# Optimization experiments

Hardware: AMD Instinct MI355X
Metric: run time of the kernel (lower is better)

The kernel has to match this reference:

```python
import jax, jax.numpy as jnp
import numpy as np

LN_EPS = 1e-5
DIM = 128
HEADS = 6
DIM_HEAD = 32
INNER = HEADS * DIM_HEAD          # 192
FF_INNER = int(DIM * 4 * 2 / 3)   # 341 (GEGLU inner dim)
LOCAL_WINDOW = 200
CACHE = 3
COMPRESS = 2
TW = LOCAL_WINDOW + CACHE         # 203
B = 2
T = 12800                         # 32 chunks of 400


def layer_norm(x, w, b):
    m = x.mean(-1, keepdims=True)
    v = ((x - m) ** 2).mean(-1, keepdims=True)
    return (x - m) / jnp.sqrt(v + LN_EPS) * w + b


def apply_rotary(q, k):
    # q, k: (b, h, n, d); standard half-rotation rotary over absolute positions
    d = q.shape[-1]
    n = q.shape[2]
    inv_freq = 1.0 / (10000.0 ** (jnp.arange(0, d, 2, dtype=jnp.float32) / d))
    freqs = jnp.arange(n, dtype=jnp.float32)[:, None] * inv_freq  # (n, d/2)
    emb = jnp.concatenate([freqs, freqs], axis=-1)                # (n, d)
    cos = jnp.cos(emb).astype(q.dtype)
    sin = jnp.sin(emb).astype(q.dtype)

    def rot_half(x):
        x1, x2 = jnp.split(x, 2, axis=-1)
        return jnp.concatenate([-x2, x1], axis=-1)

    rope = lambda x: x * cos + rot_half(x) * sin
    return rope(q), rope(k)


def local_attention(q, k, v, w):
    # causal local attention, look_backward=1 window, look_forward=0 (lucidrains LocalAttention)
    b, h, n, d = q.shape
    nw = n // w
    q, k = apply_rotary(q, k)
    qw = q.reshape(b, h, nw, w, d)

    def look_around(x):
        xw = x.reshape(b, h, nw, w, d)
        prev = jnp.pad(xw[:, :, :-1], ((0, 0), (0, 0), (1, 0), (0, 0), (0, 0)))
        return jnp.concatenate([prev, xw], axis=3)  # (b,h,nw,2w,d)

    kw = look_around(k)
    vw = look_around(v)

    t = jnp.arange(n).reshape(nw, w)
    tk_prev = jnp.pad(t[:-1], ((1, 0), (0, 0)), constant_values=-1)
    tk = jnp.concatenate([tk_prev, t], axis=1)  # (nw, 2w); -1 marks padding
    mask = (t[:, :, None] >= tk[:, None, :]) & (tk[:, None, :] >= 0)  # (nw, w, 2w)

    sim = jnp.einsum('bhwid,bhwjd->bhwij', qw, kw) * (d ** -0.5)
    neg = jnp.finfo(sim.dtype).min
    sim = jnp.where(mask[None, None], sim, neg)
    attn = jax.nn.softmax(sim, axis=-1)
    out = jnp.einsum('bhwij,bhwjd->bhwid', attn, vw)
    return out.reshape(b, h, n, d)


def local_mha(x, ln_w, ln_b, wqkv, wo, window):
    h = layer_norm(x, ln_w, ln_b)
    qkv = h @ wqkv                       # (b, n, 3*INNER)
    q, k, v = jnp.split(qkv, 3, axis=-1)

    def split_heads(t):
        bb, n, _ = t.shape
        return t.reshape(bb, n, HEADS, DIM_HEAD).transpose(0, 2, 1, 3)

    out = local_attention(split_heads(q), split_heads(k), split_heads(v), window)
    bb, hh, n, d = out.shape
    out = out.transpose(0, 2, 1, 3).reshape(bb, n, hh * d)
    return out @ wo


def feed_forward(x, ln_w, ln_b, w1, w2):
    h = layer_norm(x, ln_w, ln_b) @ w1   # (b, n, 2*FF_INNER)
    a, gate = jnp.split(h, 2, axis=-1)
    return (a * jax.nn.gelu(gate, approximate=False)) @ w2


def local_trans(x, ln1_w, ln1_b, wqkv, wo, ln2_w, ln2_b, w1, w2, window):
    n_layers = ln1_w.shape[0]
    for i in range(n_layers):
        x = x + local_mha(x, ln1_w[i], ln1_b[i], wqkv[i], wo[i], window)
        x = x + feed_forward(x, ln2_w[i], ln2_b[i], w1[i], w2[i])
    return x


def setup_inputs() -> dict:
    key = jax.random.key(0)
    ks = jax.random.split(key, 16)
    std = 0.02
    rn = lambda k, shape: jax.random.normal(k, shape, dtype=jnp.float32) * std
    inp = {
        'x': jax.random.normal(ks[0], (B, DIM, T), dtype=jnp.float32),
        'cache_token': jax.random.normal(ks[1], (1, CACHE * COMPRESS, DIM), dtype=jnp.float32),
    }
    ki = 2
    for g in ('dt', 'lt'):
        inp[g + '_ln1_w'] = jnp.ones((2, DIM), jnp.float32)
        inp[g + '_ln1_b'] = jnp.zeros((2, DIM), jnp.float32)
        inp[g + '_wqkv'] = rn(ks[ki], (2, DIM, 3 * INNER)); ki += 1
        inp[g + '_wo'] = rn(ks[ki], (2, INNER, DIM)); ki += 1
        inp[g + '_ln2_w'] = jnp.ones((2, DIM), jnp.float32)
        inp[g + '_ln2_b'] = jnp.zeros((2, DIM), jnp.float32)
        inp[g + '_w1'] = rn(ks[ki], (2, DIM, 2 * FF_INNER)); ki += 1
        inp[g + '_w2'] = rn(ks[ki], (2, FF_INNER, DIM)); ki += 1
    inp['conv_w'] = rn(ks[ki], (DIM, DIM, COMPRESS)); ki += 1
    inp['conv_b'] = jnp.zeros((DIM,), jnp.float32)
    return inp


def reference(x, cache_token,
              dt_ln1_w, dt_ln1_b, dt_wqkv, dt_wo, dt_ln2_w, dt_ln2_b, dt_w1, dt_w2,
              lt_ln1_w, lt_ln1_b, lt_wqkv, lt_wo, lt_ln2_w, lt_ln2_b, lt_w1, lt_w2,
              conv_w, conv_b):
    feat = x.transpose(0, 2, 1)                     # (B, T, C)
    b, t, c = feat.shape
    chunk = LOCAL_WINDOW * COMPRESS                 # 400
    nchunks = t // chunk
    feat = feat.reshape(b, nchunks, chunk, c)
    ct = jnp.broadcast_to(cache_token[:, None], (b, nchunks, CACHE * COMPRESS, c))
    feat = jnp.concatenate([ct, feat], axis=2)      # interleave cache tokens per chunk
    feat = feat.reshape(b, nchunks * (chunk + CACHE * COMPRESS), c)

    # DownTrans: 2-layer local transformer (window 406) + strided conv compress
    feat = local_trans(feat, dt_ln1_w, dt_ln1_b, dt_wqkv, dt_wo,
                       dt_ln2_w, dt_ln2_b, dt_w1, dt_w2, TW * COMPRESS)
    y = jax.lax.conv_general_dilated(
        feat.transpose(0, 2, 1), conv_w, (COMPRESS,), 'VALID',
        dimension_numbers=('NCH', 'OIH', 'NCH')) + conv_b[None, :, None]
    feat = y.transpose(0, 2, 1)                     # (B, n/2, C)

    # remaining depth-2 local transformer (window 203)
    feat = local_trans(feat, lt_ln1_w, lt_ln1_b, lt_wqkv, lt_wo,
                       lt_ln2_w, lt_ln2_b, lt_w1, lt_w2, TW)
    return feat
```

## Files before the change

### kernel.cpp

```cpp
#include <hip/hip_runtime.h>
#include <cstdint>
#include <cstddef>

#define DIM    128
#define HEADS  6
#define INNER  192
#define QKV3   576
#define FFI    341
#define FF2    682
#define GGP    352
#define BATCH  2
#define T_IN   12800
#define N1     12992
#define N2     6496
#define ROWS1  (BATCH * N1)
#define ROWS2  (BATCH * N2)
#define W_DT   406
#define W_LT   203

typedef unsigned short ushortT;
typedef unsigned int u32;
typedef __bf16 bf16x8 __attribute__((ext_vector_type(8)));
typedef float f32x4 __attribute__((ext_vector_type(4)));

__device__ __forceinline__ f32x4 mfma16(bf16x8 a, bf16x8 b, f32x4 c) {
  return __builtin_amdgcn_mfma_f32_16x16x32_bf16(a, b, c, 0, 0, 0);
}
__device__ __forceinline__ ushortT f2bf(float x) {
  union { __bf16 b; ushortT u; } c; c.b = (__bf16)x; return c.u;
}
__device__ __forceinline__ void async_copy16(const ushortT* g, ushortT* l) {
  __builtin_amdgcn_global_load_lds(
      (const __attribute__((address_space(1))) unsigned int*)g,
      (__attribute__((address_space(3))) unsigned int*)l, 16, 0, 0);
}

static constexpr size_t OF_FEAT = 0;
static constexpr size_t OF_H    = OF_FEAT + (size_t)ROWS1 * DIM;
static constexpr size_t OF_QKH  = OF_H + (size_t)ROWS1 * DIM / 2;
static constexpr size_t SZ_QKH  = ((size_t)(ROWS1 + 128) * 384) / 2;
static constexpr size_t OF_AO   = OF_QKH + SZ_QKH;
static constexpr size_t OF_VT   = OF_AO + (size_t)ROWS1 * INNER / 2;
static constexpr size_t SZ_VT   = ((size_t)384 * (N1 + 128)) / 2;
static constexpr size_t OF_GG   = OF_VT + SZ_VT;
static constexpr size_t OF_F2   = OF_GG + (size_t)ROWS1 * GGP / 2;
static constexpr size_t OF_WT   = OF_F2 + (size_t)ROWS2 * DIM;
static constexpr size_t WT_QKV = 0;
static constexpr size_t WT_WO  = 81920;
static constexpr size_t WT_W1  = 106496;
static constexpr size_t WT_W2  = 204800;
static constexpr size_t WT_SET = 249856;
static constexpr size_t OF_CW  = OF_WT + (4 * WT_SET) / 2 + 64;
static constexpr size_t OF_ROPE = OF_CW + (128 * 256) / 2 + 64;
static constexpr size_t OF_H2  = OF_ROPE + (size_t)N1 * 32;

__global__ void build_feat_kernel(const float* __restrict__ x,
                                  const float* __restrict__ cache,
                                  float* __restrict__ feat) {
  int idx = blockIdx.x * 256 + threadIdx.x;
  if (idx >= ROWS1 * DIM) return;
  int d = idx & 127;
  int row = idx >> 7;
  int b = row / N1;
  int i = row - b * N1;
  int c = i / 406;
  int j = i - c * 406;
  float v;
  if (j < 6) v = cache[j * DIM + d];
  else       v = x[((size_t)b * DIM + d) * T_IN + (c * 400 + j - 6)];
  feat[idx] = v;
}

__global__ __launch_bounds__(256) void ln_kernel(const float* __restrict__ x,
                                                 ushortT* __restrict__ y,
                                                 const float* __restrict__ w,
                                                 const float* __restrict__ bb,
                                                 int rows) {
  int row = blockIdx.x * 4 + (threadIdx.x >> 6);
  if (row >= rows) return;
  int lane = threadIdx.x & 63;
  const float* xr = x + (size_t)row * DIM;
  float2 v = *(const float2*)(xr + lane * 2);
  float s = v.x + v.y;
#pragma unroll
  for (int off = 32; off; off >>= 1) s += __shfl_xor(s, off);
  float mean = s * (1.0f / 128.0f);
  float dx = v.x - mean, dy = v.y - mean;
  float q = dx * dx + dy * dy;
#pragma unroll
  for (int off = 32; off; off >>= 1) q += __shfl_xor(q, off);
  float rstd = rsqrtf(q * (1.0f / 128.0f) + 1e-5f);
  float2 wv = *(const float2*)(w + lane * 2);
  float2 bv = *(const float2*)(bb + lane * 2);
  u32 packed = (u32)f2bf(dx * rstd * wv.x + bv.x) |
               ((u32)f2bf(dy * rstd * wv.y + bv.y) << 16);
  *(u32*)(y + (size_t)row * DIM + lane * 2) = packed;
}

__global__ __launch_bounds__(256) void gemm_nln(
    const ushortT* __restrict__ A, int lda,
    const ushortT* __restrict__ Wt, int ldw,
    const float* __restrict__ C, float* __restrict__ Co,
    const float* __restrict__ bias,
    int M, int Kpad, int addC,
    const float* __restrict__ lnw, const float* __restrict__ lnb,
    ushortT* __restrict__ hout, ushortT* __restrict__ bfout) {
  __shared__ ushortT As[64 * 32];
  __shared__ ushortT Bs[128 * 32];
  __shared__ float lnS[64][4];
  const int tid = threadIdx.x;
  const int wid = tid >> 6, lane = tid & 63;
  const int ck = lane & 15, quad = lane >> 4;
  const int bm = blockIdx.y * 64;
  const int wr = (wid >> 1) * 32, wc = (wid & 1) * 64;
  const int half = wid & 1;
  f32x4 acc[2][4];
#pragma unroll
  for (int t = 0; t < 2; t++)
#pragma unroll
    for (int u = 0; u < 4; u++) acc[t][u] = (f32x4){0.f, 0.f, 0.f, 0.f};

  for (int k0 = 0; k0 < Kpad; k0 += 32) {
    __syncthreads();
    {
      int idx = wid * 64 + lane;
      int row = idx >> 2, seg = (idx & 3) << 3;
      async_copy16(A + (size_t)(bm + row) * lda + k0 + seg, As + (size_t)(wid * 64) * 8);
    }
#pragma unroll
    for (int c2 = 0; c2 < 2; c2++) {
      int idx = c2 * 256 + wid * 64 + lane;
      int row = idx >> 2, seg = (idx & 3) << 3;
      async_copy16(Wt + (size_t)row * ldw + k0 + seg, Bs + (size_t)(c2 * 256 + wid * 64) * 8);
    }
    __syncthreads();
    bf16x8 af[2], bfr[4];
#pragma unroll
    for (int t = 0; t < 2; t++)
      af[t] = *(const bf16x8*)&As[(wr + t * 16 + ck) * 32 + quad * 8];
#pragma unroll
    for (int u = 0; u < 4; u++)
      bfr[u] = *(const bf16x8*)&Bs[(wc + u * 16 + ck) * 32 + quad * 8];
#pragma unroll
    for (int t = 0; t < 2; t++)
#pragma unroll
      for (int u = 0; u < 4; u++)
        acc[t][u] = mfma16(af[t], bfr[u], acc[t][u]);
  }

  float bv4[4] = {0.f, 0.f, 0.f, 0.f};
  if (bias) {
#pragma unroll
    for (int u = 0; u < 4; u++) bv4[u] = bias[wc + u * 16 + ck];
  }
  float res[2][4][4];
#pragma unroll
  for (int t = 0; t < 2; t++) {
#pragma unroll
    for (int r = 0; r < 4; r++) {
      int row = bm + wr + t * 16 + quad * 4 + r;
      const float* crow = C + (size_t)row * DIM;
#pragma unroll
      for (int u = 0; u < 4; u++) {
        int col = wc + u * 16 + ck;
        float v = acc[t][u][r] + bv4[u];
        if (addC) v += crow[col];
        res[t][r][u] = v;
      }
      if (Co) {
        float* orow = Co + (size_t)row * DIM;
#pragma unroll
        for (int u = 0; u < 4; u++) orow[wc + u * 16 + ck] = res[t][r][u];
      }
      if (bfout) {
        ushortT* brow = bfout + (size_t)row * DIM;
#pragma unroll
        for (int u = 0; u < 4; u++) brow[wc + u * 16 + ck] = f2bf(res[t][r][u]);
      }
    }
  }

  if (hout) {
#pragma unroll
    for (int t = 0; t < 2; t++) {
#pragma unroll
      for (int r = 0; r < 4; r++) {
        float s1 = ((res[t][r][0] + res[t][r][1]) + (res[t][r][2] + res[t][r][3]));
        float s2 = ((res[t][r][0] * res[t][r][0] + res[t][r][1] * res[t][r][1]) +
                    (res[t][r][2] * res[t][r][2] + res[t][r][3] * res[t][r][3]));
        s1 += __shfl_xor(s1, 1); s2 += __shfl_xor(s2, 1);
        s1 += __shfl_xor(s1, 2); s2 += __shfl_xor(s2, 2);
        s1 += __shfl_xor(s1, 4); s2 += __shfl_xor(s2, 4);
        s1 += __shfl_xor(s1, 8); s2 += __shfl_xor(s2, 8);
        if (ck == 0) {
          int rowIn = wr + t * 16 + quad * 4 + r;
          lnS[rowIn][half * 2]     = s1;
          lnS[rowIn][half * 2 + 1] = s2;
        }
      }
    }
    __syncthreads();
    float lw[4], lb[4];
#pragma unroll
    for (int u = 0; u < 4; u++) {
      lw[u] = lnw[wc + u * 16 + ck];
      lb[u] = lnb[wc + u * 16 + ck];
    }
#pragma unroll
    for (int t = 0; t < 2; t++) {
#pragma unroll
      for (int r = 0; r < 4; r++) {
        int rowIn = wr + t * 16 + quad * 4 + r;
        float S1 = lnS[rowIn][0] + lnS[rowIn][2];
        float S2 = lnS[rowIn][1] + lnS[rowIn][3];
        float mean = S1 * (1.0f / 128.0f);
        float var = S2 * (1.0f / 128.0f) - mean * mean;
        float rstd = rsqrtf(var + 1e-5f);
        ushortT* hrow = hout + (size_t)(bm + rowIn) * DIM;
#pragma unroll
        for (int u = 0; u < 4; u++) {
          int col = wc + u * 16 + ck;
          hrow[col] = f2bf((res[t][r][u] - mean) * rstd * lw[u] + lb[u]);
        }
      }
    }
  }
}

__global__ __launch_bounds__(256) void gemm_qkv(
    const ushortT* __restrict__ A,
    const ushortT* __restrict__ Wt,
    const float2* __restrict__ rope,
    ushortT* __restrict__ qkh,
    ushortT* __restrict__ vt,
    int M, int nseq, int nseqP) {
  __shared__ ushortT As[128 * 32];
  __shared__ ushortT Bs[128 * 32];
  const int tid = threadIdx.x;
  const int wid = tid >> 6, lane = tid & 63;
  const int ck = lane & 15, quad = lane >> 4;
  const int bm = blockIdx.y * 128, bn = blockIdx.x * 128;
  const int wr = (wid >> 1) * 64, wc = (wid & 1) * 64;
  f32x4 acc[4][4];
#pragma unroll
  for (int t = 0; t < 4; t++)
#pragma unroll
    for (int u = 0; u < 4; u++) acc[t][u] = (f32x4){0.f, 0.f, 0.f, 0.f};

  for (int k0 = 0; k0 < 128; k0 += 32) {
    __syncthreads();
#pragma unroll
    for (int c2 = 0; c2 < 2; c2++) {
      int idx = c2 * 256 + wid * 64 + lane;
      int row = idx >> 2, seg = (idx & 3) << 3;
      int ar = bm + row; if (ar > M - 1) ar = M - 1;
      async_copy16(A + (size_t)ar * 128 + k0 + seg, As + (size_t)(c2 * 256 + wid * 64) * 8);
      async_copy16(Wt + (size_t)(bn + row) * 128 + k0 + seg, Bs + (size_t)(c2 * 256 + wid * 64) * 8);
    }
    __syncthreads();
    bf16x8 af[4], bfr[4];
#pragma unroll
    for (int t = 0; t < 4; t++)
      af[t] = *(const bf16x8*)&As[(wr + t * 16 + ck) * 32 + quad * 8];
#pragma unroll
    for (int u = 0; u < 4; u++)
      bfr[u] = *(const bf16x8*)&Bs[(wc + u * 16 + ck) * 32 + quad * 8];
#pragma unroll
    for (int t = 0; t < 4; t++)
#pragma unroll
      for (int u = 0; u < 4; u++)
        acc[t][u] = mfma16(af[t], bfr[u], acc[t][u]);
  }

  const int s = bn + wc;
  if (s >= QKV3) return;

  if (s < 384) {
    const bool isQ = s < 192;
    const float SCq = 0.17677669529663687f * 1.4426950408889634f;
#pragma unroll
    for (int t = 0; t < 4; t++) {
#pragma unroll
      for (int r = 0; r < 4; r++) {
        int row = bm + wr + t * 16 + quad * 4 + r;
        if (row >= M) continue;
        int pos = (row >= nseq) ? row - nseq : row;
        float2 cssn = rope[pos * 16 + ck];
        float cs = cssn.x, sn = cssn.y;
        ushortT* orow = qkh + (size_t)row * 384;
#pragma unroll
        for (int u = 0; u < 4; u += 2) {
          float a0 = acc[t][u][r], a1 = acc[t][u + 1][r];
          float o0 = a0 * cs - a1 * sn;
          float o1 = a1 * cs + a0 * sn;
          if (isQ) { o0 *= SCq; o1 *= SCq; }
          int c0 = s + u * 16 + ck;
          orow[c0]      = f2bf(o0);
          orow[c0 + 16] = f2bf(o1);
        }
      }
    }
  } else {
#pragma unroll
    for (int t = 0; t < 4; t++) {
      int rowb = bm + wr + t * 16 + quad * 4;
      if (rowb >= M) continue;
      int bb = (rowb >= nseq) ? 1 : 0;
      int posb = rowb - bb * nseq;
#pragma unroll
      for (int u = 0; u < 4; u++) {
        int cv = s - 384 + u * 16 + ck;
        int hh = cv >> 5, d = cv & 31;
        ushort4 o;
        o.x = f2bf(acc[t][u][0]);
        o.y = f2bf(acc[t][u][1]);
        o.z = f2bf(acc[t][u][2]);
        o.w = f2bf(acc[t][u][3]);
        *(ushort4*)(vt + ((size_t)((bb * 6 + hh) * 32 + d)) * nseqP + posb) = o;
      }
    }
  }
}

__global__ __launch_bounds__(256) void gemm_w1g(
    const ushortT* __restrict__ A,
    const ushortT* __restrict__ Wt,
    ushortT* __restrict__ gg,
    int M) {
  __shared__ ushortT As[128 * 32];
  __shared__ ushortT Bs[128 * 32];
  const int tid = threadIdx.x;
  const int wid = tid >> 6, lane = tid & 63;
  const int ck = lane & 15, quad = lane >> 4;
  const int bm = blockIdx.y * 128, bn = blockIdx.x * 128;
  const int wr = (wid >> 1) * 64, wc = (wid & 1) * 64;
  f32x4 acc[4][4];
#pragma unroll
  for (int t = 0; t < 4; t++)
#pragma unroll
    for (int u = 0; u < 4; u++) acc[t][u] = (f32x4){0.f, 0.f, 0.f, 0.f};

  for (int k0 = 0; k0 < 128; k0 += 32) {
    __syncthreads();
#pragma unroll
    for (int c2 = 0; c2 < 2; c2++) {
      int idx = c2 * 256 + wid * 64 + lane;
      int row = idx >> 2, seg = (idx & 3) << 3;
      int ar = bm + row; if (ar > M - 1) ar = M - 1;
      async_copy16(A + (size_t)ar * 128 + k0 + seg, As + (size_t)(c2 * 256 + wid * 64) * 8);
      async_copy16(Wt + (size_t)(bn + row) * 128 + k0 + seg, Bs + (size_t)(c2 * 256 + wid * 64) * 8);
    }
    __syncthreads();
    bf16x8 af[4], bfr[4];
#pragma unroll
    for (int t = 0; t < 4; t++)
      af[t] = *(const bf16x8*)&As[(wr + t * 16 + ck) * 32 + quad * 8];
#pragma unroll
    for (int u = 0; u < 4; u++)
      bfr[u] = *(const bf16x8*)&Bs[(wc + u * 16 + ck) * 32 + quad * 8];
#pragma unroll
    for (int t = 0; t < 4; t++)
#pragma unroll
      for (int u = 0; u < 4; u++)
        acc[t][u] = mfma16(af[t], bfr[u], acc[t][u]);
  }

  const int s = bn + wc;
  if (s >= 704) return;
#pragma unroll
  for (int t = 0; t < 4; t++) {
#pragma unroll
    for (int r = 0; r < 4; r++) {
      int row = bm + wr + t * 16 + quad * 4 + r;
      if (row >= M) continue;
      ushortT* orow = gg + (size_t)row * GGP;
#pragma unroll
      for (int u = 0; u < 4; u += 2) {
        float a  = acc[t][u][r];
        float gt = acc[t][u + 1][r];
        float ge = 0.5f * gt * (1.0f + erff(gt * 0.70710678118654752f));
        int p = ((s + u * 16) >> 5) * 16 + ck;
        orow[p] = f2bf(a * ge);
      }
    }
  }
}

__global__ __launch_bounds__(256) void attn_kernel(
    const ushortT* __restrict__ qkh, const ushortT* __restrict__ vt,
    ushortT* __restrict__ out, int nseq, int nseqP, int w, int nw, int qgroups) {
  __shared__ __align__(16) ushortT Ks[2][64 * 32];
  __shared__ __align__(16) ushortT Vs[2][32 * 64];

  const int bx = blockIdx.x;
  const int c = bx % nw;
  const int g = (qgroups - 1) - bx / nw;
  const int h = blockIdx.y;
  const int b = blockIdx.z;
  const int tid = threadIdx.x;
  const int wv = tid >> 6;
  const int lane = tid & 63;
  const int ck = lane & 15;
  const int quad = lane >> 4;

  const ushortT* gq = qkh + (size_t)b * nseq * 384;
  const ushortT* gv = vt + ((size_t)(b * 6 + h) * 32) * nseqP;
  const int cw = c * w;
  const int q0 = g * 64;
  const int qt = q0 + wv * 16;
  const bool wave_on = qt < w;

  const int j0 = (c > 0) ? (c - 1) * w : 0;
  const int jend_block = cw + min(q0 + 63, w - 1) + 1;
  const int jend_wave = wave_on ? (cw + min(qt + 15, w - 1) + 1) : 0;
  const int ntiles = (jend_block - j0 + 63) >> 6;

  bf16x8 qf;
  {
    int qrow = cw + min(qt + ck, w - 1);
    qf = *(const bf16x8*)(gq + (size_t)qrow * 384 + h * 32 + quad * 8);
  }

  const int krow = tid >> 2, kch = tid & 3;
  const int krho = ((krow >> 5) << 5) | (((krow >> 2) & 1) << 4) |
                   (((krow >> 3) & 3) << 2) | (krow & 3);
  const int kslot = krho * 4 + kch;
  const int kphys = kslot ^ ((kslot >> 3) & 7);
  const ushortT* ksrc = gq + (size_t)krow * 384 + 192 + h * 32 + kch * 8;
  const int vphys = tid ^ ((tid >> 3) & 7);
  const ushortT* vsrc = gv + (size_t)(tid >> 3) * nseqP + (tid & 7) * 8;

  const int kbase = ((4 * ck + quad) ^ (ck >> 1)) * 8;
  const int p0 = ((8 * ck + quad) ^ (ck & 7)) * 8;
  const int p1 = p0 ^ 32;

  f32x4 olo = {0.f, 0.f, 0.f, 0.f};
  f32x4 ohi = {0.f, 0.f, 0.f, 0.f};
  f32x4 accl = {0.f, 0.f, 0.f, 0.f};
  bf16x8 onesf;
  {
    union { u32 u[4]; bf16x8 v; } o_;
    o_.u[0] = o_.u[1] = o_.u[2] = o_.u[3] = 0x3F803F80u;
    onesf = o_.v;
  }

  auto tileoff = [&](int t) -> int { return j0 + 64 * min(t, ntiles - 1); };

  float4 kX, vX, kY, vY;
  {
    float4 k0 = *(const float4*)(ksrc + (size_t)j0 * 384);
    float4 v0 = *(const float4*)(vsrc + j0);
    *(float4*)&Ks[0][(size_t)kphys * 8] = k0;
    *(float4*)&Vs[0][(size_t)vphys * 8] = v0;
    kX = *(const float4*)(ksrc + (size_t)tileoff(1) * 384);
    vX = *(const float4*)(vsrc + tileoff(1));
    kY = *(const float4*)(ksrc + (size_t)tileoff(2) * 384);
    vY = *(const float4*)(vsrc + tileoff(2));
  }

  auto compute = [&](const ushortT* KsB, const ushortT* VsB, int tb) {
    if (tb >= jend_wave) return;
    bf16x8 kf0 = *(const bf16x8*)&KsB[kbase];
    bf16x8 kf1 = *(const bf16x8*)&KsB[kbase + 512];
    bf16x8 kf2 = *(const bf16x8*)&KsB[kbase + 1024];
    bf16x8 kf3 = *(const bf16x8*)&KsB[kbase + 1536];
    bf16x8 vlo0 = *(const bf16x8*)&VsB[p0];
    bf16x8 vlo1 = *(const bf16x8*)&VsB[p1];
    bf16x8 vhi0 = *(const bf16x8*)&VsB[p0 + 1024];
    bf16x8 vhi1 = *(const bf16x8*)&VsB[p1 + 1024];
    f32x4 z = {0.f, 0.f, 0.f, 0.f};
    f32x4 s0 = mfma16(kf0, qf, z);
    f32x4 s1 = mfma16(kf1, qf, z);
    f32x4 s2 = mfma16(kf2, qf, z);
    f32x4 s3 = mfma16(kf3, qf, z);
    if (tb + 63 > cw + qt) {
      int q = cw + qt + ck;
      int kb = tb + 8 * quad;
#pragma unroll
      for (int r = 0; r < 4; r++) {
        if (kb + r > q)      s0[r] = -__builtin_inff();
        if (kb + 4 + r > q)  s1[r] = -__builtin_inff();
        if (kb + 32 + r > q) s2[r] = -__builtin_inff();
        if (kb + 36 + r > q) s3[r] = -__builtin_inff();
      }
    }
    float e00 = exp2f(s0[0]), e01 = exp2f(s0[1]), e02 = exp2f(s0[2]), e03 = exp2f(s0[3]);
    float e10 = exp2f(s1[0]), e11 = exp2f(s1[1]), e12 = exp2f(s1[2]), e13 = exp2f(s1[3]);
    float e20 = exp2f(s2[0]), e21 = exp2f(s2[1]), e22 = exp2f(s2[2]), e23 = exp2f(s2[3]);
    float e30 = exp2f(s3[0]), e31 = exp2f(s3[1]), e32 = exp2f(s3[2]), e33 = exp2f(s3[3]);
    union { bf16x8 v; u32 u[4]; } pa0, pa1;
    pa0.u[0] = (u32)f2bf(e00) | ((u32)f2bf(e01) << 16);
    pa0.u[1] = (u32)f2bf(e02) | ((u32)f2bf(e03) << 16);
    pa0.u[2] = (u32)f2bf(e10) | ((u32)f2bf(e11) << 16);
    pa0.u[3] = (u32)f2bf(e12) | ((u32)f2bf(e13) << 16);
    pa1.u[0] = (u32)f2bf(e20) | ((u32)f2bf(e21) << 16);
    pa1.u[1] = (u32)f2bf(e22) | ((u32)f2bf(e23) << 16);
    pa1.u[2] = (u32)f2bf(e30) | ((u32)f2bf(e31) << 16);
    pa1.u[3] = (u32)f2bf(e32) | ((u32)f2bf(e33) << 16);
    olo  = mfma16(pa0.v, vlo0, olo);
    olo  = mfma16(pa1.v, vlo1, olo);
    ohi  = mfma16(pa0.v, vhi0, ohi);
    ohi  = mfma16(pa1.v, vhi1, ohi);
    accl = mfma16(pa0.v, onesf, accl);
    accl = mfma16(pa1.v, onesf, accl);
  };

  for (int i = 0; i < ntiles; i += 2) {
    __syncthreads();
    *(float4*)&Ks[1][(size_t)kphys * 8] = kX;
    *(float4*)&Vs[1][(size_t)vphys * 8] = vX;
    kX = *(const float4*)(ksrc + (size_t)tileoff(i + 3) * 384);
    vX = *(const float4*)(vsrc + tileoff(i + 3));
    compute(Ks[0], Vs[0], j0 + i * 64);

    __syncthreads();
    *(float4*)&Ks[0][(size_t)kphys * 8] = kY;
    *(float4*)&Vs[0][(size_t)vphys * 8] = vY;
    kY = *(const float4*)(ksrc + (size_t)tileoff(i + 4) * 384);
    vY = *(const float4*)(vsrc + tileoff(i + 4));
    compute(Ks[1], Vs[1], j0 + (i + 1) * 64);
  }

  if (wave_on) {
#pragma unroll
    for (int r = 0; r < 4; r++) {
      int qi = qt + quad * 4 + r;
      if (qi < w) {
        float invr = 1.0f / accl[r];
        ushortT* orow = out + ((size_t)b * nseq + cw + qi) * INNER + h * 32;
        orow[ck]      = f2bf(olo[r] * invr);
        orow[ck + 16] = f2bf(ohi[r] * invr);
      }
    }
  }
}

__global__ void wconvert_all_kernel(
    const float* __restrict__ dq, const float* __restrict__ dwo,
    const float* __restrict__ dw1, const float* __restrict__ dw2,
    const float* __restrict__ lq, const float* __restrict__ lwo,
    const float* __restrict__ lw1, const float* __restrict__ lw2,
    const float* __restrict__ convw,
    ushortT* __restrict__ wt, ushortT* __restrict__ cwt,
    float2* __restrict__ rope) {
  int idx = blockIdx.x * 256 + threadIdx.x;
  const int TOTW = 4 * (int)WT_SET;
  const int CWN = 128 * 256;
  if (idx < TOTW) {
    int s = idx / (int)WT_SET;
    int rem = idx - s * (int)WT_SET;
    int lyr = s & 1;
    const float* Wq = ((s < 2) ? dq : lq) + (size_t)lyr * DIM * QKV3;
    const float* Wo = ((s < 2) ? dwo : lwo) + (size_t)lyr * INNER * DIM;
    const float* W1 = ((s < 2) ? dw1 : lw1) + (size_t)lyr * DIM * FF2;
    const float* W2 = ((s < 2) ? dw2 : lw2) + (size_t)lyr * FFI * DIM;
    float v = 0.f;
    if (rem < (int)WT_WO) {
      int n = rem >> 7, k = rem & 127;
      if (n < QKV3) v = Wq[(size_t)k * QKV3 + n];
    } else if (rem < (int)WT_W1) {
      int r = rem - (int)WT_WO;
      int n = r / INNER, k = r - n * INNER;
      v = Wo[(size_t)k * DIM + n];
    } else if (rem < (int)WT_W2) {
      int r = rem - (int)WT_W1;
      int n = r >> 7, k = r & 127;
      if (n < 704) {
        int blk = n >> 5, wi = n & 31;
        int p = blk * 16 + (wi & 15);
        if (p < FFI) {
          int src = (wi < 16) ? p : FFI + p;
          v = W1[(size_t)k * FF2 + src];
        }
      }
    } else {
      int r = rem - (int)WT_W2;
      int n = r / GGP, k = r - n * GGP;
      if (k < FFI) v = W2[(size_t)k * DIM + n];
    }
    wt[idx] = f2bf(v);
  } else if (idx < TOTW + CWN) {
    int r = idx - TOTW;
    int o = r >> 8, k = r & 255;
    int kk = k >> 7, i = k & 127;
    cwt[r] = f2bf(convw[((size_t)o * DIM + i) * 2 + kk]);
  } else {
    int r = idx - TOTW - CWN;
    if (r < N1 * 16) {
      int pos = r >> 4, k = r & 15;
      float invf = 1.0f / powf(10000.0f, (float)k * (1.0f / 16.0f));
      float sn, cs;
      sincosf((float)pos * invf, &sn, &cs);
      rope[r] = make_float2(cs, sn);
    }
  }
}

static void run_layer(float* F, float* Fout, ushortT* hbuf, ushortT* qkh, ushortT* vtb,
                      ushortT* attnb, ushortT* ggb, const ushortT* wt,
                      const float2* rope,
                      int M, int nseq, int w,
                      const float* ln2w, const float* ln2b,
                      const float* nlnw, const float* nlnb,
                      ushortT* w2bf, hipStream_t stream) {
  int nseqP = nseq + 128;
  int gy = (M + 127) / 128;
  int gy64 = M / 64;
  gemm_qkv<<<dim3(5, gy), 256, 0, stream>>>(hbuf, wt + WT_QKV, rope, qkh, vtb, M, nseq, nseqP);
  int nw = nseq / w;
  int qgroups = (w + 63) / 64;
  attn_kernel<<<dim3(nw * qgroups, HEADS, BATCH), 256, 0, stream>>>(qkh, vtb, attnb,
                                                                    nseq, nseqP, w, nw, qgroups);
  gemm_nln<<<dim3(1, gy64), 256, 0, stream>>>(attnb, INNER, wt + WT_WO, INNER, F, F,
                                              nullptr, M, INNER, 1, ln2w, ln2b,
                                              hbuf, nullptr);
  gemm_w1g<<<dim3(6, gy), 256, 0, stream>>>(hbuf, wt + WT_W1, ggb, M);
  gemm_nln<<<dim3(1, gy64), 256, 0, stream>>>(ggb, GGP, wt + WT_W2, GGP, F, Fout,
                                              nullptr, M, GGP, 1, nlnw, nlnb,
                                              nlnw ? hbuf : (ushortT*)nullptr, w2bf);
}

extern "C" void kernel_launch(void* const* d_in, const int* in_sizes, int n_in,
                              void* d_out, int out_size, void* d_ws, size_t ws_size,
                              hipStream_t stream) {
  const float* x        = (const float*)d_in[0];
  const float* cache    = (const float*)d_in[1];
  const float* dt_ln1_w = (const float*)d_in[2];
  const float* dt_ln1_b = (const float*)d_in[3];
  const float* dt_wqkv  = (const float*)d_in[4];
  const float* dt_wo    = (const float*)d_in[5];
  const float* dt_ln2_w = (const float*)d_in[6];
  const float* dt_ln2_b = (const float*)d_in[7];
  const float* dt_w1    = (const float*)d_in[8];
  const float* dt_w2    = (const float*)d_in[9];
  const float* lt_ln1_w = (const float*)d_in[10];
  const float* lt_ln1_b = (const float*)d_in[11];
  const float* lt_wqkv  = (const float*)d_in[12];
  const float* lt_wo    = (const float*)d_in[13];
  const float* lt_ln2_w = (const float*)d_in[14];
  const float* lt_ln2_b = (const float*)d_in[15];
  const float* lt_w1    = (const float*)d_in[16];
  const float* lt_w2    = (const float*)d_in[17];
  const float* conv_w   = (const float*)d_in[18];
  const float* conv_b   = (const float*)d_in[19];

  float* ws     = (float*)d_ws;
  float* feat   = ws + OF_FEAT;
  ushortT* h    = (ushortT*)(ws + OF_H);
  ushortT* qkh  = (ushortT*)(ws + OF_QKH);
  ushortT* attnb= (ushortT*)(ws + OF_AO);
  ushortT* vtb  = (ushortT*)(ws + OF_VT);
  ushortT* ggb  = (ushortT*)(ws + OF_GG);
  float* feat2  = ws + OF_F2;
  ushortT* wt   = (ushortT*)(ws + OF_WT);
  ushortT* cwt  = (ushortT*)(ws + OF_CW);
  float2* rope  = (float2*)(ws + OF_ROPE);
  ushortT* h2   = (ushortT*)(ws + OF_H2);
  float* outf   = (float*)d_out;

  {
    int total = 4 * (int)WT_SET + 128 * 256 + N1 * 16;
    wconvert_all_kernel<<<(total + 255) / 256, 256, 0, stream>>>(
        dt_wqkv, dt_wo, dt_w1, dt_w2, lt_wqkv, lt_wo, lt_w1, lt_w2,
        conv_w, wt, cwt, rope);
  }

  build_feat_kernel<<<(ROWS1 * DIM + 255) / 256, 256, 0, stream>>>(x, cache, feat);
  ln_kernel<<<ROWS1 / 4, 256, 0, stream>>>(feat, h, dt_ln1_w, dt_ln1_b, ROWS1);

  run_layer(feat, feat, h, qkh, vtb, attnb, ggb, wt + 0 * WT_SET, rope,
            ROWS1, N1, W_DT,
            dt_ln2_w, dt_ln2_b, dt_ln1_w + DIM, dt_ln1_b + DIM, nullptr, stream);
  run_layer(feat, nullptr, h, qkh, vtb, attnb, ggb, wt + 1 * WT_SET, rope,
            ROWS1, N1, W_DT,
            dt_ln2_w + DIM, dt_ln2_b + DIM, nullptr, nullptr, h, stream);

  gemm_nln<<<dim3(1, ROWS2 / 64), 256, 0, stream>>>(h, 256, cwt, 256,
                                                    feat2, feat2, conv_b,
                                                    ROWS2, 256, 0,
                                                    lt_ln1_w, lt_ln1_b, h2, nullptr);

  run_layer(feat2, feat2, h2, qkh, vtb, attnb, ggb, wt + 2 * WT_SET, rope,
            ROWS2, N2, W_LT,
            lt_ln2_w, lt_ln2_b, lt_ln1_w + DIM, lt_ln1_b + DIM, nullptr, stream);
  run_layer(feat2, outf, h2, qkh, vtb, attnb, ggb, wt + 3 * WT_SET, rope,
            ROWS2, N2, W_LT,
            lt_ln2_w + DIM, lt_ln2_b + DIM, nullptr, nullptr, nullptr, stream);
}
```

Before: 542.4 us.

## Process full attention window per block with 8 waves and 4 query fragments

The attention kernel now launches one 512-thread block per window chunk instead of one 256-thread block per 64-query group. Each wave handles up to four 16-row query fragments, so every K/V tile loaded into shared memory is reused by all queries in the window rather than reloaded per query group. K and V loading is split across the two halves of the block. This cuts redundant global K/V traffic and block count, but it raises register pressure (four sets of accumulators), can leave waves idle when the window does not fill all fragments, and reduces the number of blocks in flight.

```diff
diff --git a/kernel.cpp b/kernel.cpp
--- a/kernel.cpp
+++ b/kernel.cpp
@@ -386,15 +386,13 @@
   }
 }
 
-__global__ __launch_bounds__(256) void attn_kernel(
+__global__ __launch_bounds__(512) void attn_kernel(
     const ushortT* __restrict__ qkh, const ushortT* __restrict__ vt,
-    ushortT* __restrict__ out, int nseq, int nseqP, int w, int nw, int qgroups) {
+    ushortT* __restrict__ out, int nseq, int nseqP, int w, int nw) {
   __shared__ __align__(16) ushortT Ks[2][64 * 32];
   __shared__ __align__(16) ushortT Vs[2][32 * 64];
 
-  const int bx = blockIdx.x;
-  const int c = bx % nw;
-  const int g = (qgroups - 1) - bx / nw;
+  const int c = blockIdx.x;
   const int h = blockIdx.y;
   const int b = blockIdx.z;
   const int tid = threadIdx.x;
@@ -406,37 +404,60 @@
   const ushortT* gq = qkh + (size_t)b * nseq * 384;
   const ushortT* gv = vt + ((size_t)(b * 6 + h) * 32) * nseqP;
   const int cw = c * w;
-  const int q0 = g * 64;
-  const int qt = q0 + wv * 16;
-  const bool wave_on = qt < w;
-
   const int j0 = (c > 0) ? (c - 1) * w : 0;
-  const int jend_block = cw + min(q0 + 63, w - 1) + 1;
-  const int jend_wave = wave_on ? (cw + min(qt + 15, w - 1) + 1) : 0;
-  const int ntiles = (jend_block - j0 + 63) >> 6;
-
-  bf16x8 qf;
-  {
-    int qrow = cw + min(qt + ck, w - 1);
-    qf = *(const bf16x8*)(gq + (size_t)qrow * 384 + h * 32 + quad * 8);
-  }
-
-  const int krow = tid >> 2, kch = tid & 3;
-  const int krho = ((krow >> 5) << 5) | (((krow >> 2) & 1) << 4) |
-                   (((krow >> 3) & 3) << 2) | (krow & 3);
-  const int kslot = krho * 4 + kch;
-  const int kphys = kslot ^ ((kslot >> 3) & 7);
-  const ushortT* ksrc = gq + (size_t)krow * 384 + 192 + h * 32 + kch * 8;
-  const int vphys = tid ^ ((tid >> 3) & 7);
-  const ushortT* vsrc = gv + (size_t)(tid >> 3) * nseqP + (tid & 7) * 8;
+  const int ntiles = (cw + w - j0 + 63) >> 6;
+
+  int q0f[4], jf[4];
+  bool fact[4];
+#pragma unroll
+  for (int f = 0; f < 4; f++) {
+    q0f[f] = 16 * wv + 128 * f;
+    fact[f] = q0f[f] < w;
+    jf[f] = fact[f] ? (cw + min(q0f[f] + 15, w - 1) + 1) : 0;
+  }
+  const int jfmax = max(max(jf[0], jf[1]), max(jf[2], jf[3]));
+
+  bf16x8 qfr[4];
+#pragma unroll
+  for (int f = 0; f < 4; f++) {
+    if (fact[f]) {
+      int qrow = cw + min(q0f[f] + ck, w - 1);
+      qfr[f] = *(const bf16x8*)(gq + (size_t)qrow * 384 + h * 32 + quad * 8);
+    }
+  }
+
+  const bool isK = tid < 256;
+  const int st = isK ? tid : (tid - 256);
+  int phys;
+  const ushortT* src;
+  size_t step64;
+  if (isK) {
+    int krow = st >> 2, kch = st & 3;
+    int krho = ((krow >> 5) << 5) | (((krow >> 2) & 1) << 4) |
+               (((krow >> 3) & 3) << 2) | (krow & 3);
+    int kslot = krho * 4 + kch;
+    phys = kslot ^ ((kslot >> 3) & 7);
+    src = gq + (size_t)(j0 + krow) * 384 + 192 + h * 32 + kch * 8;
+    step64 = (size_t)64 * 384;
+  } else {
+    phys = st ^ ((st >> 3) & 7);
+    src = gv + (size_t)(st >> 3) * nseqP + (st & 7) * 8 + j0;
+    step64 = 64;
+  }
+  ushortT* dst0 = (isK ? &Ks[0][0] : &Vs[0][0]) + (size_t)phys * 8;
+  ushortT* dst1 = (isK ? &Ks[1][0] : &Vs[1][0]) + (size_t)phys * 8;
 
   const int kbase = ((4 * ck + quad) ^ (ck >> 1)) * 8;
   const int p0 = ((8 * ck + quad) ^ (ck & 7)) * 8;
   const int p1 = p0 ^ 32;
 
-  f32x4 olo = {0.f, 0.f, 0.f, 0.f};
-  f32x4 ohi = {0.f, 0.f, 0.f, 0.f};
-  f32x4 accl = {0.f, 0.f, 0.f, 0.f};
+  f32x4 olo[4], ohi[4], accl[4];
+#pragma unroll
+  for (int f = 0; f < 4; f++) {
+    olo[f] = (f32x4){0.f, 0.f, 0.f, 0.f};
+    ohi[f] = (f32x4){0.f, 0.f, 0.f, 0.f};
+    accl[f] = (f32x4){0.f, 0.f, 0.f, 0.f};
+  }
   bf16x8 onesf;
   {
     union { u32 u[4]; bf16x8 v; } o_;
@@ -444,22 +465,20 @@
     onesf = o_.v;
   }
 
-  auto tileoff = [&](int t) -> int { return j0 + 64 * min(t, ntiles - 1); };
-
-  float4 kX, vX, kY, vY;
+  auto ld = [&](int t) -> float4 {
+    return *(const float4*)(src + (size_t)min(t, ntiles - 1) * step64);
+  };
+
+  float4 rX, rY;
   {
-    float4 k0 = *(const float4*)(ksrc + (size_t)j0 * 384);
-    float4 v0 = *(const float4*)(vsrc + j0);
-    *(float4*)&Ks[0][(size_t)kphys * 8] = k0;
-    *(float4*)&Vs[0][(size_t)vphys * 8] = v0;
-    kX = *(const float4*)(ksrc + (size_t)tileoff(1) * 384);
-    vX = *(const float4*)(vsrc + tileoff(1));
-    kY = *(const float4*)(ksrc + (size_t)tileoff(2) * 384);
-    vY = *(const float4*)(vsrc + tileoff(2));
+    float4 r0 = ld(0);
+    *(float4*)dst0 = r0;
+    rX = ld(1);
+    rY = ld(2);
   }
 
   auto compute = [&](const ushortT* KsB, const ushortT* VsB, int tb) {
-    if (tb >= jend_wave) return;
+    if (tb >= jfmax) return;
     bf16x8 kf0 = *(const bf16x8*)&KsB[kbase];
     bf16x8 kf1 = *(const bf16x8*)&KsB[kbase + 512];
     bf16x8 kf2 = *(const bf16x8*)&KsB[kbase + 1024];
@@ -469,67 +488,69 @@
     bf16x8 vhi0 = *(const bf16x8*)&VsB[p0 + 1024];
     bf16x8 vhi1 = *(const bf16x8*)&VsB[p1 + 1024];
     f32x4 z = {0.f, 0.f, 0.f, 0.f};
-    f32x4 s0 = mfma16(kf0, qf, z);
-    f32x4 s1 = mfma16(kf1, qf, z);
-    f32x4 s2 = mfma16(kf2, qf, z);
-    f32x4 s3 = mfma16(kf3, qf, z);
-    if (tb + 63 > cw + qt) {
-      int q = cw + qt + ck;
-      int kb = tb + 8 * quad;
-#pragma unroll
-      for (int r = 0; r < 4; r++) {
-        if (kb + r > q)      s0[r] = -__builtin_inff();
-        if (kb + 4 + r > q)  s1[r] = -__builtin_inff();
-        if (kb + 32 + r > q) s2[r] = -__builtin_inff();
-        if (kb + 36 + r > q) s3[r] = -__builtin_inff();
-      }
-    }
-    float e00 = exp2f(s0[0]), e01 = exp2f(s0[1]), e02 = exp2f(s0[2]), e03 = exp2f(s0[3]);
-    float e10 = exp2f(s1[0]), e11 = exp2f(s1[1]), e12 = exp2f(s1[2]), e13 = exp2f(s1[3]);
-    float e20 = exp2f(s2[0]), e21 = exp2f(s2[1]), e22 = exp2f(s2[2]), e23 = exp2f(s2[3]);
-    float e30 = exp2f(s3[0]), e31 = exp2f(s3[1]), e32 = exp2f(s3[2]), e33 = exp2f(s3[3]);
-    union { bf16x8 v; u32 u[4]; } pa0, pa1;
-    pa0.u[0] = (u32)f2bf(e00) | ((u32)f2bf(e01) << 16);
-    pa0.u[1] = (u32)f2bf(e02) | ((u32)f2bf(e03) << 16);
-    pa0.u[2] = (u32)f2bf(e10) | ((u32)f2bf(e11) << 16);
-    pa0.u[3] = (u32)f2bf(e12) | ((u32)f2bf(e13) << 16);
-    pa1.u[0] = (u32)f2bf(e20) | ((u32)f2bf(e21) << 16);
-    pa1.u[1] = (u32)f2bf(e22) | ((u32)f2bf(e23) << 16);
-    pa1.u[2] = (u32)f2bf(e30) | ((u32)f2bf(e31) << 16);
-    pa1.u[3] = (u32)f2bf(e32) | ((u32)f2bf(e33) << 16);
-    olo  = mfma16(pa0.v, vlo0, olo);
-    olo  = mfma16(pa1.v, vlo1, olo);
-    ohi  = mfma16(pa0.v, vhi0, ohi);
-    ohi  = mfma16(pa1.v, vhi1, ohi);
-    accl = mfma16(pa0.v, onesf, accl);
-    accl = mfma16(pa1.v, onesf, accl);
+#pragma unroll
+    for (int f = 0; f < 4; f++) {
+      if (tb >= jf[f]) continue;
+      f32x4 s0 = mfma16(kf0, qfr[f], z);
+      f32x4 s1 = mfma16(kf1, qfr[f], z);
+      f32x4 s2 = mfma16(kf2, qfr[f], z);
+      f32x4 s3 = mfma16(kf3, qfr[f], z);
+      if (tb + 63 > cw + q0f[f]) {
+        int q = cw + q0f[f] + ck;
+        int kb = tb + 8 * quad;
+#pragma unroll
+        for (int r = 0; r < 4; r++) {
+          if (kb + r > q)      s0[r] = -__builtin_inff();
+          if (kb + 4 + r > q)  s1[r] = -__builtin_inff();
+          if (kb + 32 + r > q) s2[r] = -__builtin_inff();
+          if (kb + 36 + r > q) s3[r] = -__builtin_inff();
+        }
+      }
+      float e00 = exp2f(s0[0]), e01 = exp2f(s0[1]), e02 = exp2f(s0[2]), e03 = exp2f(s0[3]);
+      float e10 = exp2f(s1[0]), e11 = exp2f(s1[1]), e12 = exp2f(s1[2]), e13 = exp2f(s1[3]);
+      float e20 = exp2f(s2[0]), e21 = exp2f(s2[1]), e22 = exp2f(s2[2]), e23 = exp2f(s2[3]);
+      float e30 = exp2f(s3[0]), e31 = exp2f(s3[1]), e32 = exp2f(s3[2]), e33 = exp2f(s3[3]);
+      union { bf16x8 v; u32 u[4]; } pa0, pa1;
+      pa0.u[0] = (u32)f2bf(e00) | ((u32)f2bf(e01) << 16);
+      pa0.u[1] = (u32)f2bf(e02) | ((u32)f2bf(e03) << 16);
+      pa0.u[2] = (u32)f2bf(e10) | ((u32)f2bf(e11) << 16);
+      pa0.u[3] = (u32)f2bf(e12) | ((u32)f2bf(e13) << 16);
+      pa1.u[0] = (u32)f2bf(e20) | ((u32)f2bf(e21) << 16);
+      pa1.u[1] = (u32)f2bf(e22) | ((u32)f2bf(e23) << 16);
+      pa1.u[2] = (u32)f2bf(e30) | ((u32)f2bf(e31) << 16);
+      pa1.u[3] = (u32)f2bf(e32) | ((u32)f2bf(e33) << 16);
+      olo[f]  = mfma16(pa0.v, vlo0, olo[f]);
+      olo[f]  = mfma16(pa1.v, vlo1, olo[f]);
+      ohi[f]  = mfma16(pa0.v, vhi0, ohi[f]);
+      ohi[f]  = mfma16(pa1.v, vhi1, ohi[f]);
+      accl[f] = mfma16(pa0.v, onesf, accl[f]);
+      accl[f] = mfma16(pa1.v, onesf, accl[f]);
+    }
   };
 
   for (int i = 0; i < ntiles; i += 2) {
     __syncthreads();
-    *(float4*)&Ks[1][(size_t)kphys * 8] = kX;
-    *(float4*)&Vs[1][(size_t)vphys * 8] = vX;
-    kX = *(const float4*)(ksrc + (size_t)tileoff(i + 3) * 384);
-    vX = *(const float4*)(vsrc + tileoff(i + 3));
+    *(float4*)dst1 = rX;
+    rX = ld(i + 3);
     compute(Ks[0], Vs[0], j0 + i * 64);
 
     __syncthreads();
-    *(float4*)&Ks[0][(size_t)kphys * 8] = kY;
-    *(float4*)&Vs[0][(size_t)vphys * 8] = vY;
-    kY = *(const float4*)(ksrc + (size_t)tileoff(i + 4) * 384);
-    vY = *(const float4*)(vsrc + tileoff(i + 4));
+    *(float4*)dst0 = rY;
+    rY = ld(i + 4);
     compute(Ks[1], Vs[1], j0 + (i + 1) * 64);
   }
 
-  if (wave_on) {
+#pragma unroll
+  for (int f = 0; f < 4; f++) {
+    if (!fact[f]) continue;
 #pragma unroll
     for (int r = 0; r < 4; r++) {
-      int qi = qt + quad * 4 + r;
+      int qi = q0f[f] + quad * 4 + r;
       if (qi < w) {
-        float invr = 1.0f / accl[r];
+        float invr = 1.0f / accl[f][r];
         ushortT* orow = out + ((size_t)b * nseq + cw + qi) * INNER + h * 32;
-        orow[ck]      = f2bf(olo[r] * invr);
-        orow[ck + 16] = f2bf(ohi[r] * invr);
+        orow[ck]      = f2bf(olo[f][r] * invr);
+        orow[ck + 16] = f2bf(ohi[f][r] * invr);
       }
     }
   }
@@ -608,9 +629,8 @@
   int gy64 = M / 64;
   gemm_qkv<<<dim3(5, gy), 256, 0, stream>>>(hbuf, wt + WT_QKV, rope, qkh, vtb, M, nseq, nseqP);
   int nw = nseq / w;
-  int qgroups = (w + 63) / 64;
-  attn_kernel<<<dim3(nw * qgroups, HEADS, BATCH), 256, 0, stream>>>(qkh, vtb, attnb,
-                                                                    nseq, nseqP, w, nw, qgroups);
+  attn_kernel<<<dim3(nw, HEADS, BATCH), 512, 0, stream>>>(qkh, vtb, attnb,
+                                                          nseq, nseqP, w, nw);
   gemm_nln<<<dim3(1, gy64), 256, 0, stream>>>(attnb, INNER, wt + WT_WO, INNER, F, F,
                                               nullptr, M, INNER, 1, ln2w, ln2b,
                                               hbuf, nullptr);
```

Measured after the change: 566.9 us. 1.05x slower.

## Load attention K/V fragments directly from global into registers, drop LDS staging

Applied to the files above, without the earlier changes.

The attention kernel no longer stages K and V tiles through double-buffered shared memory with block-wide barriers. Each wave now loads its MFMA operand fragments straight from global memory into registers, with a two-deep register prefetch. Inactive waves exit early, and each wave limits its tile count to its own causal extent. This removes __syncthreads and LDS traffic and lets waves run independently. The cost is redundant global loads across the four waves and less coalesced access to K rows, which rely on cache hits.

```diff
diff --git a/kernel.cpp b/kernel.cpp
--- a/kernel.cpp
+++ b/kernel.cpp
@@ -389,9 +389,6 @@
 __global__ __launch_bounds__(256) void attn_kernel(
     const ushortT* __restrict__ qkh, const ushortT* __restrict__ vt,
     ushortT* __restrict__ out, int nseq, int nseqP, int w, int nw, int qgroups) {
-  __shared__ __align__(16) ushortT Ks[2][64 * 32];
-  __shared__ __align__(16) ushortT Vs[2][32 * 64];
-
   const int bx = blockIdx.x;
   const int c = bx % nw;
   const int g = (qgroups - 1) - bx / nw;
@@ -403,17 +400,16 @@
   const int ck = lane & 15;
   const int quad = lane >> 4;
 
-  const ushortT* gq = qkh + (size_t)b * nseq * 384;
-  const ushortT* gv = vt + ((size_t)(b * 6 + h) * 32) * nseqP;
   const int cw = c * w;
   const int q0 = g * 64;
   const int qt = q0 + wv * 16;
-  const bool wave_on = qt < w;
-
+  if (qt >= w) return;
+
+  const ushortT* gq = qkh + (size_t)b * nseq * 384;
+  const ushortT* gv = vt + ((size_t)(b * 6 + h) * 32) * nseqP;
   const int j0 = (c > 0) ? (c - 1) * w : 0;
-  const int jend_block = cw + min(q0 + 63, w - 1) + 1;
-  const int jend_wave = wave_on ? (cw + min(qt + 15, w - 1) + 1) : 0;
-  const int ntiles = (jend_block - j0 + 63) >> 6;
+  const int jend = cw + min(qt + 15, w - 1) + 1;
+  const int ntiles = (jend - j0 + 63) >> 6;
 
   bf16x8 qf;
   {
@@ -421,18 +417,9 @@
     qf = *(const bf16x8*)(gq + (size_t)qrow * 384 + h * 32 + quad * 8);
   }
 
-  const int krow = tid >> 2, kch = tid & 3;
-  const int krho = ((krow >> 5) << 5) | (((krow >> 2) & 1) << 4) |
-                   (((krow >> 3) & 3) << 2) | (krow & 3);
-  const int kslot = krho * 4 + kch;
-  const int kphys = kslot ^ ((kslot >> 3) & 7);
-  const ushortT* ksrc = gq + (size_t)krow * 384 + 192 + h * 32 + kch * 8;
-  const int vphys = tid ^ ((tid >> 3) & 7);
-  const ushortT* vsrc = gv + (size_t)(tid >> 3) * nseqP + (tid & 7) * 8;
-
-  const int kbase = ((4 * ck + quad) ^ (ck >> 1)) * 8;
-  const int p0 = ((8 * ck + quad) ^ (ck & 7)) * 8;
-  const int p1 = p0 ^ 32;
+  const ushortT* kb_ = gq + (size_t)(8 * (ck >> 2) + (ck & 3)) * 384 + 192 + h * 32 + quad * 8;
+  const ushortT* vb_ = gv + (size_t)ck * nseqP + quad * 8;
+  const size_t VH = (size_t)16 * nseqP;
 
   f32x4 olo = {0.f, 0.f, 0.f, 0.f};
   f32x4 ohi = {0.f, 0.f, 0.f, 0.f};
@@ -444,35 +431,29 @@
     onesf = o_.v;
   }
 
-  auto tileoff = [&](int t) -> int { return j0 + 64 * min(t, ntiles - 1); };
-
-  float4 kX, vX, kY, vY;
-  {
-    float4 k0 = *(const float4*)(ksrc + (size_t)j0 * 384);
-    float4 v0 = *(const float4*)(vsrc + j0);
-    *(float4*)&Ks[0][(size_t)kphys * 8] = k0;
-    *(float4*)&Vs[0][(size_t)vphys * 8] = v0;
-    kX = *(const float4*)(ksrc + (size_t)tileoff(1) * 384);
-    vX = *(const float4*)(vsrc + tileoff(1));
-    kY = *(const float4*)(ksrc + (size_t)tileoff(2) * 384);
-    vY = *(const float4*)(vsrc + tileoff(2));
-  }
-
-  auto compute = [&](const ushortT* KsB, const ushortT* VsB, int tb) {
-    if (tb >= jend_wave) return;
-    bf16x8 kf0 = *(const bf16x8*)&KsB[kbase];
-    bf16x8 kf1 = *(const bf16x8*)&KsB[kbase + 512];
-    bf16x8 kf2 = *(const bf16x8*)&KsB[kbase + 1024];
-    bf16x8 kf3 = *(const bf16x8*)&KsB[kbase + 1536];
-    bf16x8 vlo0 = *(const bf16x8*)&VsB[p0];
-    bf16x8 vlo1 = *(const bf16x8*)&VsB[p1];
-    bf16x8 vhi0 = *(const bf16x8*)&VsB[p0 + 1024];
-    bf16x8 vhi1 = *(const bf16x8*)&VsB[p1 + 1024];
+#define LOADK(tb, kf)                                                      \
+  {                                                                        \
+    const ushortT* p_ = kb_ + (size_t)(tb) * 384;                          \
+    kf[0] = *(const bf16x8*)(p_);                                          \
+    kf[1] = *(const bf16x8*)(p_ + (size_t)4 * 384);                        \
+    kf[2] = *(const bf16x8*)(p_ + (size_t)32 * 384);                       \
+    kf[3] = *(const bf16x8*)(p_ + (size_t)36 * 384);                       \
+  }
+#define LOADV(tb, vf)                                                      \
+  {                                                                        \
+    const ushortT* p_ = vb_ + (tb);                                        \
+    vf[0] = *(const bf16x8*)(p_);                                          \
+    vf[1] = *(const bf16x8*)(p_ + 32);                                     \
+    vf[2] = *(const bf16x8*)(p_ + VH);                                     \
+    vf[3] = *(const bf16x8*)(p_ + VH + 32);                                \
+  }
+
+  auto compute = [&](int tb, const bf16x8* kf, const bf16x8* vf) {
     f32x4 z = {0.f, 0.f, 0.f, 0.f};
-    f32x4 s0 = mfma16(kf0, qf, z);
-    f32x4 s1 = mfma16(kf1, qf, z);
-    f32x4 s2 = mfma16(kf2, qf, z);
-    f32x4 s3 = mfma16(kf3, qf, z);
+    f32x4 s0 = mfma16(kf[0], qf, z);
+    f32x4 s1 = mfma16(kf[1], qf, z);
+    f32x4 s2 = mfma16(kf[2], qf, z);
+    f32x4 s3 = mfma16(kf[3], qf, z);
     if (tb + 63 > cw + qt) {
       int q = cw + qt + ck;
       int kb = tb + 8 * quad;
@@ -497,40 +478,39 @@
     pa1.u[1] = (u32)f2bf(e22) | ((u32)f2bf(e23) << 16);
     pa1.u[2] = (u32)f2bf(e30) | ((u32)f2bf(e31) << 16);
     pa1.u[3] = (u32)f2bf(e32) | ((u32)f2bf(e33) << 16);
-    olo  = mfma16(pa0.v, vlo0, olo);
-    olo  = mfma16(pa1.v, vlo1, olo);
-    ohi  = mfma16(pa0.v, vhi0, ohi);
-    ohi  = mfma16(pa1.v, vhi1, ohi);
+    olo  = mfma16(pa0.v, vf[0], olo);
+    olo  = mfma16(pa1.v, vf[1], olo);
+    ohi  = mfma16(pa0.v, vf[2], ohi);
+    ohi  = mfma16(pa1.v, vf[3], ohi);
     accl = mfma16(pa0.v, onesf, accl);
     accl = mfma16(pa1.v, onesf, accl);
   };
 
+  bf16x8 kA[4], vA[4], kB[4], vB[4];
+  LOADK(j0, kA); LOADV(j0, vA);
   for (int i = 0; i < ntiles; i += 2) {
-    __syncthreads();
-    *(float4*)&Ks[1][(size_t)kphys * 8] = kX;
-    *(float4*)&Vs[1][(size_t)vphys * 8] = vX;
-    kX = *(const float4*)(ksrc + (size_t)tileoff(i + 3) * 384);
-    vX = *(const float4*)(vsrc + tileoff(i + 3));
-    compute(Ks[0], Vs[0], j0 + i * 64);
-
-    __syncthreads();
-    *(float4*)&Ks[0][(size_t)kphys * 8] = kY;
-    *(float4*)&Vs[0][(size_t)vphys * 8] = vY;
-    kY = *(const float4*)(ksrc + (size_t)tileoff(i + 4) * 384);
-    vY = *(const float4*)(vsrc + tileoff(i + 4));
-    compute(Ks[1], Vs[1], j0 + (i + 1) * 64);
-  }
-
-  if (wave_on) {
-#pragma unroll
-    for (int r = 0; r < 4; r++) {
-      int qi = qt + quad * 4 + r;
-      if (qi < w) {
-        float invr = 1.0f / accl[r];
-        ushortT* orow = out + ((size_t)b * nseq + cw + qi) * INNER + h * 32;
-        orow[ck]      = f2bf(olo[r] * invr);
-        orow[ck + 16] = f2bf(ohi[r] * invr);
-      }
+    {
+      int tn = j0 + 64 * min(i + 1, ntiles - 1);
+      LOADK(tn, kB); LOADV(tn, vB);
+    }
+    compute(j0 + i * 64, kA, vA);
+    {
+      int tn = j0 + 64 * min(i + 2, ntiles - 1);
+      LOADK(tn, kA); LOADV(tn, vA);
+    }
+    if (i + 1 < ntiles) compute(j0 + (i + 1) * 64, kB, vB);
+  }
+#undef LOADK
+#undef LOADV
+
+#pragma unroll
+  for (int r = 0; r < 4; r++) {
+    int qi = qt + quad * 4 + r;
+    if (qi < w) {
+      float invr = 1.0f / accl[r];
+      ushortT* orow = out + ((size_t)b * nseq + cw + qi) * INNER + h * 32;
+      orow[ck]      = f2bf(olo[r] * invr);
+      orow[ck + 16] = f2bf(ohi[r] * invr);
     }
   }
 }
```

After: 746.1 us. 37.6% more time.

## Process two 64-row query fragments per attention block to reuse K/V tiles

Applied to the files above, without the earlier changes.

Each attention block now covers 128 query rows instead of 64, with every wave holding two query fragments and two sets of accumulators. K/V tiles loaded into shared memory are reused across both fragments, which halves the number of blocks and the redundant K/V staging. Wave priority is raised during compute with s_setprio. The cost is higher register pressure, fewer blocks for parallelism, and more wasted work at window edges, where w=203 or 406 is not a multiple of 128.

```diff
diff --git a/kernel.cpp b/kernel.cpp
--- a/kernel.cpp
+++ b/kernel.cpp
@@ -406,19 +406,25 @@
   const ushortT* gq = qkh + (size_t)b * nseq * 384;
   const ushortT* gv = vt + ((size_t)(b * 6 + h) * 32) * nseqP;
   const int cw = c * w;
-  const int q0 = g * 64;
-  const int qt = q0 + wv * 16;
-  const bool wave_on = qt < w;
+  const int q0 = g * 128;
+  const int qt0 = q0 + wv * 16;
+  const int qt1 = q0 + 64 + wv * 16;
+  const bool f0on = qt0 < w;
+  const bool f1on = qt1 < w;
 
   const int j0 = (c > 0) ? (c - 1) * w : 0;
-  const int jend_block = cw + min(q0 + 63, w - 1) + 1;
-  const int jend_wave = wave_on ? (cw + min(qt + 15, w - 1) + 1) : 0;
+  const int jend_block = cw + min(q0 + 127, w - 1) + 1;
+  const int jf0 = f0on ? (cw + min(qt0 + 15, w - 1) + 1) : 0;
+  const int jf1 = f1on ? (cw + min(qt1 + 15, w - 1) + 1) : 0;
+  const int jmax = max(jf0, jf1);
   const int ntiles = (jend_block - j0 + 63) >> 6;
 
-  bf16x8 qf;
+  bf16x8 qf0, qf1;
   {
-    int qrow = cw + min(qt + ck, w - 1);
-    qf = *(const bf16x8*)(gq + (size_t)qrow * 384 + h * 32 + quad * 8);
+    int qrow0 = cw + min(qt0 + ck, w - 1);
+    qf0 = *(const bf16x8*)(gq + (size_t)qrow0 * 384 + h * 32 + quad * 8);
+    int qrow1 = cw + min(qt1 + ck, w - 1);
+    qf1 = *(const bf16x8*)(gq + (size_t)qrow1 * 384 + h * 32 + quad * 8);
   }
 
   const int krow = tid >> 2, kch = tid & 3;
@@ -434,9 +440,8 @@
   const int p0 = ((8 * ck + quad) ^ (ck & 7)) * 8;
   const int p1 = p0 ^ 32;
 
-  f32x4 olo = {0.f, 0.f, 0.f, 0.f};
-  f32x4 ohi = {0.f, 0.f, 0.f, 0.f};
-  f32x4 accl = {0.f, 0.f, 0.f, 0.f};
+  f32x4 olo0 = {0.f, 0.f, 0.f, 0.f}, ohi0 = {0.f, 0.f, 0.f, 0.f}, accl0 = {0.f, 0.f, 0.f, 0.f};
+  f32x4 olo1 = {0.f, 0.f, 0.f, 0.f}, ohi1 = {0.f, 0.f, 0.f, 0.f}, accl1 = {0.f, 0.f, 0.f, 0.f};
   bf16x8 onesf;
   {
     union { u32 u[4]; bf16x8 v; } o_;
@@ -458,16 +463,10 @@
     vY = *(const float4*)(vsrc + tileoff(2));
   }
 
-  auto compute = [&](const ushortT* KsB, const ushortT* VsB, int tb) {
-    if (tb >= jend_wave) return;
-    bf16x8 kf0 = *(const bf16x8*)&KsB[kbase];
-    bf16x8 kf1 = *(const bf16x8*)&KsB[kbase + 512];
-    bf16x8 kf2 = *(const bf16x8*)&KsB[kbase + 1024];
-    bf16x8 kf3 = *(const bf16x8*)&KsB[kbase + 1536];
-    bf16x8 vlo0 = *(const bf16x8*)&VsB[p0];
-    bf16x8 vlo1 = *(const bf16x8*)&VsB[p1];
-    bf16x8 vhi0 = *(const bf16x8*)&VsB[p0 + 1024];
-    bf16x8 vhi1 = *(const bf16x8*)&VsB[p1 + 1024];
+  auto frag = [&](int tb, const bf16x8& qf, int qt,
+                  const bf16x8& kf0, const bf16x8& kf1, const bf16x8& kf2, const bf16x8& kf3,
+                  const bf16x8& vlo0, const bf16x8& vlo1, const bf16x8& vhi0, const bf16x8& vhi1,
+                  f32x4& olo, f32x4& ohi, f32x4& accl) {
     f32x4 z = {0.f, 0.f, 0.f, 0.f};
     f32x4 s0 = mfma16(kf0, qf, z);
     f32x4 s1 = mfma16(kf1, qf, z);
@@ -505,6 +504,24 @@
     accl = mfma16(pa1.v, onesf, accl);
   };
 
+  auto compute = [&](const ushortT* KsB, const ushortT* VsB, int tb) {
+    if (tb >= jmax) return;
+    __builtin_amdgcn_s_setprio(1);
+    bf16x8 kf0 = *(const bf16x8*)&KsB[kbase];
+    bf16x8 kf1 = *(const bf16x8*)&KsB[kbase + 512];
+    bf16x8 kf2 = *(const bf16x8*)&KsB[kbase + 1024];
+    bf16x8 kf3 = *(const bf16x8*)&KsB[kbase + 1536];
+    bf16x8 vlo0 = *(const bf16x8*)&VsB[p0];
+    bf16x8 vlo1 = *(const bf16x8*)&VsB[p1];
+    bf16x8 vhi0 = *(const bf16x8*)&VsB[p0 + 1024];
+    bf16x8 vhi1 = *(const bf16x8*)&VsB[p1 + 1024];
+    if (tb < jf0)
+      frag(tb, qf0, qt0, kf0, kf1, kf2, kf3, vlo0, vlo1, vhi0, vhi1, olo0, ohi0, accl0);
+    if (tb < jf1)
+      frag(tb, qf1, qt1, kf0, kf1, kf2, kf3, vlo0, vlo1, vhi0, vhi1, olo1, ohi1, accl1);
+    __builtin_amdgcn_s_setprio(0);
+  };
+
   for (int i = 0; i < ntiles; i += 2) {
     __syncthreads();
     *(float4*)&Ks[1][(size_t)kphys * 8] = kX;
@@ -521,15 +538,27 @@
     compute(Ks[1], Vs[1], j0 + (i + 1) * 64);
   }
 
-  if (wave_on) {
+  if (f0on) {
 #pragma unroll
     for (int r = 0; r < 4; r++) {
-      int qi = qt + quad * 4 + r;
+      int qi = qt0 + quad * 4 + r;
       if (qi < w) {
-        float invr = 1.0f / accl[r];
+        float invr = 1.0f / accl0[r];
         ushortT* orow = out + ((size_t)b * nseq + cw + qi) * INNER + h * 32;
-        orow[ck]      = f2bf(olo[r] * invr);
-        orow[ck + 16] = f2bf(ohi[r] * invr);
+        orow[ck]      = f2bf(olo0[r] * invr);
+        orow[ck + 16] = f2bf(ohi0[r] * invr);
+      }
+    }
+  }
+  if (f1on) {
+#pragma unroll
+    for (int r = 0; r < 4; r++) {
+      int qi = qt1 + quad * 4 + r;
+      if (qi < w) {
+        float invr = 1.0f / accl1[r];
+        ushortT* orow = out + ((size_t)b * nseq + cw + qi) * INNER + h * 32;
+        orow[ck]      = f2bf(olo1[r] * invr);
+        orow[ck + 16] = f2bf(ohi1[r] * invr);
       }
     }
   }
@@ -608,7 +637,7 @@
   int gy64 = M / 64;
   gemm_qkv<<<dim3(5, gy), 256, 0, stream>>>(hbuf, wt + WT_QKV, rope, qkh, vtb, M, nseq, nseqP);
   int nw = nseq / w;
-  int qgroups = (w + 63) / 64;
+  int qgroups = (w + 127) / 128;
   attn_kernel<<<dim3(nw * qgroups, HEADS, BATCH), 256, 0, stream>>>(qkh, vtb, attnb,
                                                                     nseq, nseqP, w, nw, qgroups);
   gemm_nln<<<dim3(1, gy64), 256, 0, stream>>>(attnb, INNER, wt + WT_WO, INNER, F, F,
```

New measurement: 552.2 us. Within noise of the previous version (+1.8%).
